# Kernel tuning notes

Hardware: AMD Instinct MI355X
Metric: run time of the kernel (lower is better)

The kernel has to match this reference:

```python
import jax, jax.numpy as jnp
import numpy as np

EXTENTS = (1, 2, 2)   # local half-window per (s, h, w) axis -> window 3x5x5 = 75
HEADS = 8
DIM_HEAD = 32
MASK_VALUE = -1e9


def unfold_axis(x, axis, size):
    # sliding windows of `size` along `axis` (stride 1), window dim appended last
    n = x.shape[axis] - size + 1
    idx = jnp.arange(n)[:, None] + jnp.arange(size)[None, :]
    out = jnp.take(x, idx, axis=axis)          # (..., n, size, ...)
    return jnp.moveaxis(out, axis + 1, -1)     # (..., n, ..., size)


def unfold3d(x, extents):
    # mimics torch x.unfold over dims 1,2,3; appends 3 window dims at the end
    for i in range(3):
        x = unfold_axis(x, i + 1, 2 * extents[i] + 1)
    return x


def local3d_attention(x, q, wq, wk, wv, wo, bo):
    b, s, h, w, dim = q.shape
    heads, dh = HEADS, DIM_HEAD
    inner = heads * dh
    scale = dh ** -0.5
    es, eh, ew = EXTENTS

    k = x @ wk.T                               # (b,s,h,w,inner)
    v = x @ wv.T
    qp = q @ wq.T

    pad_cfg = ((0, 0), (es, es), (eh, eh), (ew, ew), (0, 0))
    N = b * s * h * w
    # unfold -> (b,s,h,w,inner,ks,kh,kw); inner is head-major: (heads, dh)
    kwin = unfold3d(jnp.pad(k, pad_cfg), EXTENTS).reshape(N, heads, dh, -1)
    vwin = unfold3d(jnp.pad(v, pad_cfg), EXTENTS).reshape(N, heads, dh, -1)
    win = kwin.shape[-1]

    # mask: True where window position falls in the zero padding
    m = jnp.zeros((1, s, h, w), dtype=bool)
    m = jnp.pad(m, ((0, 0), (es, es), (eh, eh), (ew, ew)), constant_values=True)
    m = unfold3d(m, EXTENTS).reshape(s * h * w, win)
    m = jnp.tile(m, (b, 1))

    qn = qp.reshape(N, heads, dh)
    dots = jnp.einsum('nhd,nhdk->nhk', qn, kwin) * scale
    dots = jnp.where(m[:, None, :], MASK_VALUE, dots)
    attn = jax.nn.softmax(dots, axis=-1)
    out = jnp.einsum('nhk,nhdk->nhd', attn, vwin).reshape(b, s, h, w, inner)
    return out @ wo.T + bo                     # (b,s,h,w,dim)


def setup_inputs() -> dict:
    key = jax.random.key(0)
    ks = jax.random.split(key, 6)
    b, s, h, w, dim = 2, 8, 32, 16, 256
    inner = HEADS * DIM_HEAD
    sc_in = dim ** -0.5
    sc_out = inner ** -0.5
    return {
        'x': jax.random.normal(ks[0], (b, s, h, w, dim), jnp.float32),
        'q': jax.random.normal(ks[1], (b, s, h, w, dim), jnp.float32),
        'wq': jax.random.normal(ks[2], (inner, dim), jnp.float32) * sc_in,
        'wk': jax.random.normal(ks[3], (inner, dim), jnp.float32) * sc_in,
        'wv': jax.random.normal(ks[4], (inner, dim), jnp.float32) * sc_in,
        'wo': jax.random.normal(ks[5], (dim, inner), jnp.float32) * sc_out,
        'bo': jnp.zeros((dim,), jnp.float32),
    }


def reference(x, q, wq, wk, wv, wo, bo):
    return local3d_attention(x, q, wq, wk, wv, wo, bo)
```

## Files before the change

kernel.cpp:

```cpp
#include <hip/hip_runtime.h>
#include <hip/hip_bf16.h>
#include <math.h>

#define HEADS 8
#define DH 32
#define DIM 256
#define INNER 256
#define B_ 2
#define S_ 8
#define H_ 32
#define W_ 16
#define NTOK (B_*S_*H_*W_)

#define VHSTRIDE (512*32*16)
#define AOP 264

typedef _Float16 h16;
typedef h16 half8 __attribute__((ext_vector_type(8)));
typedef h16 half4 __attribute__((ext_vector_type(4)));
typedef float f32x4 __attribute__((ext_vector_type(4)));

#define QSCALE 0.17677669529663687f

#define GBM 128
#define GBN 64
#define GBK 32
#define GPITCH 40

__device__ __forceinline__ uint4 cvt8(const float4 a, const float4 b) {
    union { h16 h[8]; uint4 u; } p;
    p.h[0] = (h16)a.x; p.h[1] = (h16)a.y; p.h[2] = (h16)a.z; p.h[3] = (h16)a.w;
    p.h[4] = (h16)b.x; p.h[5] = (h16)b.y; p.h[6] = (h16)b.z; p.h[7] = (h16)b.w;
    return p.u;
}

template <int OUT_MODE>
__device__ __forceinline__ void mfma_gemm_tile_t(
    const float* __restrict__ A, const float* __restrict__ W,
    void* __restrict__ outv, int m0, int j0, float oscale,
    h16* aT, h16* bT)
{
    const int tid  = threadIdx.x;
    const int lane = tid & 63;
    const int wid  = tid >> 6;
    const int wr   = wid >> 1;
    const int wc   = wid & 1;
    const int r    = lane & 15;
    const int g    = lane >> 4;

    f32x4 acc[4][2];
    #pragma unroll
    for (int i = 0; i < 4; ++i)
        #pragma unroll
        for (int j = 0; j < 2; ++j)
            acc[i][j] = (f32x4){0.f, 0.f, 0.f, 0.f};

    const int arow  = tid >> 1;
    const int ahalf = (tid & 1) * 16;
    const int brow  = (tid & 127) >> 1;
    const bool doB  = tid < 128;

    for (int k0 = 0; k0 < DIM; k0 += GBK) {
        {
            const float* src = A + (size_t)(m0 + arow) * DIM + k0 + ahalf;
            const float4 u0 = *(const float4*)(src + 0);
            const float4 u1 = *(const float4*)(src + 4);
            const float4 u2 = *(const float4*)(src + 8);
            const float4 u3 = *(const float4*)(src + 12);
            *(uint4*)(aT + arow * GPITCH + ahalf + 0) = cvt8(u0, u1);
            *(uint4*)(aT + arow * GPITCH + ahalf + 8) = cvt8(u2, u3);
        }
        if (doB) {
            const float* src = W + (size_t)(j0 + brow) * DIM + k0 + ahalf;
            const float4 u0 = *(const float4*)(src + 0);
            const float4 u1 = *(const float4*)(src + 4);
            const float4 u2 = *(const float4*)(src + 8);
            const float4 u3 = *(const float4*)(src + 12);
            *(uint4*)(bT + brow * GPITCH + ahalf + 0) = cvt8(u0, u1);
            *(uint4*)(bT + brow * GPITCH + ahalf + 8) = cvt8(u2, u3);
        }
        __syncthreads();

        half8 af[4], bf[2];
        #pragma unroll
        for (int fr = 0; fr < 4; ++fr)
            af[fr] = *(const half8*)(aT + (wr * 64 + fr * 16 + r) * GPITCH + g * 8);
        #pragma unroll
        for (int fc = 0; fc < 2; ++fc)
            bf[fc] = *(const half8*)(bT + (wc * 32 + fc * 16 + r) * GPITCH + g * 8);

        #pragma unroll
        for (int fr = 0; fr < 4; ++fr)
            #pragma unroll
            for (int fc = 0; fc < 2; ++fc)
                acc[fr][fc] = __builtin_amdgcn_mfma_f32_16x16x32_f16(
                    af[fr], bf[fc], acc[fr][fc], 0, 0, 0);
        __syncthreads();
    }

    #pragma unroll
    for (int fr = 0; fr < 4; ++fr) {
        #pragma unroll
        for (int fc = 0; fc < 2; ++fc) {
            const int col = j0 + wc * 32 + fc * 16 + r;
            if constexpr (OUT_MODE == 4) {
                const int hd = col >> 5, d = col & 31;
                const int rowb = m0 + wr * 64 + fr * 16 + g * 4;
                union { h16 h[4]; uint2 u; } p;
                #pragma unroll
                for (int i = 0; i < 4; ++i) p.h[i] = (h16)(acc[fr][fc][i] * oscale);
                h16* dst = (h16*)outv + ((size_t)hd * 512 + (rowb >> 4)) * 512
                           + d * 16 + (rowb & 15);
                *(uint2*)dst = p.u;
            } else {
                const int hd = col >> 5, d = col & 31;
                #pragma unroll
                for (int i = 0; i < 4; ++i) {
                    const int row = m0 + wr * 64 + fr * 16 + g * 4 + i;
                    ((h16*)outv)[((size_t)hd * NTOK + row) * DH + d] =
                        (h16)(acc[fr][fc][i] * oscale);
                }
            }
        }
    }
}

__global__ __launch_bounds__(256) void proj_kernel(
    const float* __restrict__ x, const float* __restrict__ q,
    const float* __restrict__ wq, const float* __restrict__ wk,
    const float* __restrict__ wv, const float* __restrict__ wo,
    h16* __restrict__ qk, h16* __restrict__ vtb, h16* __restrict__ wof16)
{
    __shared__ h16 aT[GBM * GPITCH];
    __shared__ h16 bT[GBN * GPITCH];

    const int seg = blockIdx.y >> 2;
    const int jt  = blockIdx.y & 3;

    if (seg == 3) {
        const int idx = (blockIdx.x * 256 + threadIdx.x) * 4;
        const float4 v = *(const float4*)(wo + idx);
        union { h16 h[4]; uint2 u; } p;
        p.h[0] = (h16)v.x; p.h[1] = (h16)v.y;
        p.h[2] = (h16)v.z; p.h[3] = (h16)v.w;
        *(uint2*)(wof16 + idx) = p.u;
        return;
    }

    const float* A = (seg == 0) ? q : x;
    const float* W = (seg == 0) ? wq : ((seg == 1) ? wk : wv);

    if (seg == 2) {
        mfma_gemm_tile_t<4>(A, W, vtb, blockIdx.x * GBM, jt * GBN, 1.0f, aT, bT);
    } else {
        h16* outp = qk + (size_t)seg * HEADS * NTOK * DH;
        const float sc = (seg == 0) ? QSCALE : 1.0f;
        mfma_gemm_tile_t<3>(A, W, outp, blockIdx.x * GBM, jt * GBN, sc, aT, bT);
    }
}

__global__ __launch_bounds__(512, 4) void attn_kernel(
    const h16* __restrict__ qk, const h16* __restrict__ vtb,
    const h16* __restrict__ wof16, const float* __restrict__ bo,
    float* __restrict__ out)
{
    __shared__ h16 ao_lds[16][AOP];

    const int tid  = threadIdx.x;
    const int lane = tid & 63;
    const int wid  = __builtin_amdgcn_readfirstlane(tid >> 6);
    const int xr   = blockIdx.x;
    const int r    = ((xr & 7) << 6) | (xr >> 3);
    const int head = wid;
    const int h = r & 31, s = (r >> 5) & 7, b = r >> 8;
    const int n_base = r * 16;
    const int c = lane & 15, g = lane >> 4;

    const h16* qb = qk + (size_t)head * NTOK * DH;
    const h16* kb = qk + (size_t)(HEADS + head) * NTOK * DH;
    const h16* vb = vtb + (size_t)head * VHSTRIDE;

    int   tokb[16];
    float kill[16];
    #pragma unroll
    for (int t = 0; t < 16; ++t) {
        const int ds = t / 5, hh = t - 5 * ds;
        const int s2 = s + ds - 1;
        const int h2 = h + hh - 2;
        const bool inb = (t < 15) && ((unsigned)s2 < 8u) && ((unsigned)h2 < 32u);
        const int s2c = min(max(s2, 0), 7);
        const int h2c = min(max(h2, 0), 31);
        tokb[t] = ((b * 8 + s2c) * 32 + h2c) * 16;
        kill[t] = inb ? __builtin_inff() : -1e30f;
    }

    const half8 qf = *(const half8*)(qb + (size_t)(n_base + c) * DH + g * 8);

    f32x4 dots[16];
    #pragma unroll
    for (int t = 0; t < 16; ++t) {
        const half8 kf = *(const half8*)(kb + (size_t)(tokb[t] + c) * DH + g * 8);
        dots[t] = __builtin_amdgcn_mfma_f32_16x16x32_f16(
            kf, qf, (f32x4){0.f, 0.f, 0.f, 0.f}, 0, 0, 0);
    }

    union u2h4 { uint2 u2; half4 hv; } vpre[16];
    #pragma unroll
    for (int t = 0; t < 16; ++t) {
        const int bv = tokb[t] >> 4;
        vpre[t].u2 = *(const uint2*)(vb + (size_t)bv * 512 + c * 16 + 4 * g);
    }

    bool okw[4];
    #pragma unroll
    for (int i = 0; i < 4; ++i) {
        const int w2 = 4 * g + i;
        okw[i] = ((unsigned)(w2 - c + 2) <= 4u);
    }
    float mx = -1e30f;
    #pragma unroll
    for (int t = 0; t < 16; ++t) {
        const float kl = kill[t];
        #pragma unroll
        for (int i = 0; i < 4; ++i) {
            float dv = okw[i] ? dots[t][i] : -1e30f;
            dv = fminf(dv, kl);
            dots[t][i] = dv;
            mx = fmaxf(mx, dv);
        }
    }
    mx = fmaxf(mx, __shfl_xor(mx, 16));
    mx = fmaxf(mx, __shfl_xor(mx, 32));

    float sum = 0.f;
    int d0[16], d1[16];
    #pragma unroll
    for (int t = 0; t < 16; ++t) {
        const float e0v = __expf(dots[t][0] - mx);
        const float e1v = __expf(dots[t][1] - mx);
        const float e2v = __expf(dots[t][2] - mx);
        const float e3v = __expf(dots[t][3] - mx);
        sum += (e0v + e1v) + (e2v + e3v);
        union { h16 hh2[2]; int u; } p0, p1;
        p0.hh2[0] = (h16)e0v; p0.hh2[1] = (h16)e1v;
        p1.hh2[0] = (h16)e2v; p1.hh2[1] = (h16)e3v;
        d0[t] = p0.u; d1[t] = p1.u;
    }
    sum += __shfl_xor(sum, 16);
    sum += __shfl_xor(sum, 32);
    const float inv = 1.f / sum;
    float invq[4];
    #pragma unroll
    for (int i = 0; i < 4; ++i) invq[i] = __shfl(inv, 4 * g + i);

    f32x4 o0 = (f32x4){0.f,0.f,0.f,0.f};
    f32x4 o1 = (f32x4){0.f,0.f,0.f,0.f};
    #pragma unroll
    for (int t = 0; t < 16; ++t) {
        union { int u[2]; half4 hv; } pa;
        pa.u[0] = d0[t]; pa.u[1] = d1[t];

        const int bv = tokb[t] >> 4;
        union u2h4 v1;
        v1.u2 = *(const uint2*)(vb + (size_t)bv * 512 + (c + 16) * 16 + 4 * g);

        o0 = __builtin_amdgcn_mfma_f32_16x16x16f16(pa.hv, vpre[t].hv, o0, 0, 0, 0);
        o1 = __builtin_amdgcn_mfma_f32_16x16x16f16(pa.hv, v1.hv, o1, 0, 0, 0);
    }

    #pragma unroll
    for (int i = 0; i < 4; ++i) {
        ao_lds[4 * g + i][head * DH + c]      = (h16)(o0[i] * invq[i]);
        ao_lds[4 * g + i][head * DH + 16 + c] = (h16)(o1[i] * invq[i]);
    }
    __syncthreads();

    const int n0 = wid * 32;
    f32x4 oacc[2];
    oacc[0] = (f32x4){0.f,0.f,0.f,0.f};
    oacc[1] = (f32x4){0.f,0.f,0.f,0.f};
    #pragma unroll
    for (int kc = 0; kc < 8; ++kc) {
        const half8 af = *(const half8*)&ao_lds[c][kc * 32 + g * 8];
        #pragma unroll
        for (int nt = 0; nt < 2; ++nt) {
            const half8 bf = *(const half8*)(wof16
                + (size_t)(n0 + nt * 16 + c) * DIM + kc * 32 + g * 8);
            oacc[nt] = __builtin_amdgcn_mfma_f32_16x16x32_f16(af, bf, oacc[nt], 0, 0, 0);
        }
    }
    #pragma unroll
    for (int nt = 0; nt < 2; ++nt) {
        const int col = n0 + nt * 16 + c;
        const float badd = bo[col];
        #pragma unroll
        for (int i = 0; i < 4; ++i) {
            const int row = n_base + 4 * g + i;
            out[(size_t)row * INNER + col] = oacc[nt][i] + badd;
        }
    }
}

extern "C" void kernel_launch(void* const* d_in, const int* in_sizes, int n_in,
                              void* d_out, int out_size, void* d_ws, size_t ws_size,
                              hipStream_t stream) {
    const float* x  = (const float*)d_in[0];
    const float* q  = (const float*)d_in[1];
    const float* wq = (const float*)d_in[2];
    const float* wk = (const float*)d_in[3];
    const float* wv = (const float*)d_in[4];
    const float* wo = (const float*)d_in[5];
    const float* bo = (const float*)d_in[6];
    float* out = (float*)d_out;

    h16* qk    = (h16*)d_ws;
    h16* vtb   = qk + (size_t)2 * HEADS * NTOK * DH;
    h16* wof16 = vtb + (size_t)HEADS * VHSTRIDE;

    dim3 g1(NTOK / GBM, 13);
    proj_kernel<<<g1, 256, 0, stream>>>(x, q, wq, wk, wv, wo, qk, vtb, wof16);

    attn_kernel<<<512, 512, 0, stream>>>(qk, vtb, wof16, bo, out);
}
```

Baseline: 43.44 us.

## Retile projection GEMM to 64x256 blocks covering full output width

Each projection block now computes a 64-row by full 256-column output tile, so the A (activation) tile is read and converted only once per block instead of once per 64-column strip. The grid changes from 64x13 blocks to 128x4, and each wave now owns 64 columns with a 4x4 MFMA accumulator set. This cuts redundant global reads of x and q, but each block now loads the full 256-row weight slice every k-step, and the wo conversion segment uses narrower float2 loads. The added per-thread accumulator registers may also reduce occupancy.

```diff
diff --git a/kernel.cpp b/kernel.cpp
--- a/kernel.cpp
+++ b/kernel.cpp
@@ -22,10 +22,9 @@
 
 #define QSCALE 0.17677669529663687f
 
-#define GBM 128
-#define GBN 64
-#define GBK 32
 #define GPITCH 40
+#define PBM 64
+#define PBK 32
 
 __device__ __forceinline__ uint4 cvt8(const float4 a, const float4 b) {
     union { h16 h[8]; uint4 u; } p;
@@ -34,34 +33,49 @@
     return p.u;
 }
 
-template <int OUT_MODE>
-__device__ __forceinline__ void mfma_gemm_tile_t(
-    const float* __restrict__ A, const float* __restrict__ W,
-    void* __restrict__ outv, int m0, int j0, float oscale,
-    h16* aT, h16* bT)
+__global__ __launch_bounds__(256) void proj_kernel(
+    const float* __restrict__ x, const float* __restrict__ q,
+    const float* __restrict__ wq, const float* __restrict__ wk,
+    const float* __restrict__ wv, const float* __restrict__ wo,
+    h16* __restrict__ qk, h16* __restrict__ vtb, h16* __restrict__ wof16)
 {
-    const int tid  = threadIdx.x;
+    __shared__ h16 aT[PBM * GPITCH];
+    __shared__ h16 bT[256 * GPITCH];
+
+    const int seg = blockIdx.y;
+    const int tid = threadIdx.x;
+
+    if (seg == 3) {
+        const int idx = (blockIdx.x * 256 + tid) * 2;
+        const float2 v = *(const float2*)(wo + idx);
+        union { h16 h[2]; uint u; } p;
+        p.h[0] = (h16)v.x; p.h[1] = (h16)v.y;
+        *(uint*)(wof16 + idx) = p.u;
+        return;
+    }
+
+    const float* A = (seg == 0) ? q : x;
+    const float* W = (seg == 0) ? wq : ((seg == 1) ? wk : wv);
+    const float sc = (seg == 0) ? QSCALE : 1.0f;
+    const int m0 = blockIdx.x * PBM;
+
     const int lane = tid & 63;
     const int wid  = tid >> 6;
-    const int wr   = wid >> 1;
-    const int wc   = wid & 1;
     const int r    = lane & 15;
     const int g    = lane >> 4;
 
-    f32x4 acc[4][2];
+    f32x4 acc[4][4];
     #pragma unroll
     for (int i = 0; i < 4; ++i)
         #pragma unroll
-        for (int j = 0; j < 2; ++j)
+        for (int j = 0; j < 4; ++j)
             acc[i][j] = (f32x4){0.f, 0.f, 0.f, 0.f};
 
     const int arow  = tid >> 1;
     const int ahalf = (tid & 1) * 16;
-    const int brow  = (tid & 127) >> 1;
-    const bool doB  = tid < 128;
-
-    for (int k0 = 0; k0 < DIM; k0 += GBK) {
-        {
+
+    for (int k0 = 0; k0 < DIM; k0 += PBK) {
+        if (tid < 128) {
             const float* src = A + (size_t)(m0 + arow) * DIM + k0 + ahalf;
             const float4 u0 = *(const float4*)(src + 0);
             const float4 u1 = *(const float4*)(src + 4);
@@ -70,29 +84,35 @@
             *(uint4*)(aT + arow * GPITCH + ahalf + 0) = cvt8(u0, u1);
             *(uint4*)(aT + arow * GPITCH + ahalf + 8) = cvt8(u2, u3);
         }
-        if (doB) {
-            const float* src = W + (size_t)(j0 + brow) * DIM + k0 + ahalf;
+        {
+            const float* src = W + (size_t)tid * DIM + k0;
             const float4 u0 = *(const float4*)(src + 0);
             const float4 u1 = *(const float4*)(src + 4);
             const float4 u2 = *(const float4*)(src + 8);
             const float4 u3 = *(const float4*)(src + 12);
-            *(uint4*)(bT + brow * GPITCH + ahalf + 0) = cvt8(u0, u1);
-            *(uint4*)(bT + brow * GPITCH + ahalf + 8) = cvt8(u2, u3);
+            const float4 u4 = *(const float4*)(src + 16);
+            const float4 u5 = *(const float4*)(src + 20);
+            const float4 u6 = *(const float4*)(src + 24);
+            const float4 u7 = *(const float4*)(src + 28);
+            *(uint4*)(bT + tid * GPITCH + 0)  = cvt8(u0, u1);
+            *(uint4*)(bT + tid * GPITCH + 8)  = cvt8(u2, u3);
+            *(uint4*)(bT + tid * GPITCH + 16) = cvt8(u4, u5);
+            *(uint4*)(bT + tid * GPITCH + 24) = cvt8(u6, u7);
         }
         __syncthreads();
 
-        half8 af[4], bf[2];
+        half8 af[4], bf[4];
         #pragma unroll
         for (int fr = 0; fr < 4; ++fr)
-            af[fr] = *(const half8*)(aT + (wr * 64 + fr * 16 + r) * GPITCH + g * 8);
-        #pragma unroll
-        for (int fc = 0; fc < 2; ++fc)
-            bf[fc] = *(const half8*)(bT + (wc * 32 + fc * 16 + r) * GPITCH + g * 8);
+            af[fr] = *(const half8*)(aT + (fr * 16 + r) * GPITCH + g * 8);
+        #pragma unroll
+        for (int fc = 0; fc < 4; ++fc)
+            bf[fc] = *(const half8*)(bT + (wid * 64 + fc * 16 + r) * GPITCH + g * 8);
 
         #pragma unroll
         for (int fr = 0; fr < 4; ++fr)
             #pragma unroll
-            for (int fc = 0; fc < 2; ++fc)
+            for (int fc = 0; fc < 4; ++fc)
                 acc[fr][fc] = __builtin_amdgcn_mfma_f32_16x16x32_f16(
                     af[fr], bf[fc], acc[fr][fc], 0, 0, 0);
         __syncthreads();
@@ -101,61 +121,27 @@
     #pragma unroll
     for (int fr = 0; fr < 4; ++fr) {
         #pragma unroll
-        for (int fc = 0; fc < 2; ++fc) {
-            const int col = j0 + wc * 32 + fc * 16 + r;
-            if constexpr (OUT_MODE == 4) {
-                const int hd = col >> 5, d = col & 31;
-                const int rowb = m0 + wr * 64 + fr * 16 + g * 4;
+        for (int fc = 0; fc < 4; ++fc) {
+            const int col = wid * 64 + fc * 16 + r;
+            const int hd = col >> 5, d = col & 31;
+            if (seg == 2) {
+                const int rowb = m0 + fr * 16 + g * 4;
                 union { h16 h[4]; uint2 u; } p;
                 #pragma unroll
-                for (int i = 0; i < 4; ++i) p.h[i] = (h16)(acc[fr][fc][i] * oscale);
-                h16* dst = (h16*)outv + ((size_t)hd * 512 + (rowb >> 4)) * 512
+                for (int i = 0; i < 4; ++i) p.h[i] = (h16)acc[fr][fc][i];
+                h16* dst = vtb + ((size_t)hd * 512 + (rowb >> 4)) * 512
                            + d * 16 + (rowb & 15);
                 *(uint2*)dst = p.u;
             } else {
-                const int hd = col >> 5, d = col & 31;
+                h16* outp = qk + (size_t)seg * HEADS * NTOK * DH;
                 #pragma unroll
                 for (int i = 0; i < 4; ++i) {
-                    const int row = m0 + wr * 64 + fr * 16 + g * 4 + i;
-                    ((h16*)outv)[((size_t)hd * NTOK + row) * DH + d] =
-                        (h16)(acc[fr][fc][i] * oscale);
+                    const int row = m0 + fr * 16 + g * 4 + i;
+                    outp[((size_t)hd * NTOK + row) * DH + d] =
+                        (h16)(acc[fr][fc][i] * sc);
                 }
             }
         }
-    }
-}
-
-__global__ __launch_bounds__(256) void proj_kernel(
-    const float* __restrict__ x, const float* __restrict__ q,
-    const float* __restrict__ wq, const float* __restrict__ wk,
-    const float* __restrict__ wv, const float* __restrict__ wo,
-    h16* __restrict__ qk, h16* __restrict__ vtb, h16* __restrict__ wof16)
-{
-    __shared__ h16 aT[GBM * GPITCH];
-    __shared__ h16 bT[GBN * GPITCH];
-
-    const int seg = blockIdx.y >> 2;
-    const int jt  = blockIdx.y & 3;
-
-    if (seg == 3) {
-        const int idx = (blockIdx.x * 256 + threadIdx.x) * 4;
-        const float4 v = *(const float4*)(wo + idx);
-        union { h16 h[4]; uint2 u; } p;
-        p.h[0] = (h16)v.x; p.h[1] = (h16)v.y;
-        p.h[2] = (h16)v.z; p.h[3] = (h16)v.w;
-        *(uint2*)(wof16 + idx) = p.u;
-        return;
-    }
-
-    const float* A = (seg == 0) ? q : x;
-    const float* W = (seg == 0) ? wq : ((seg == 1) ? wk : wv);
-
-    if (seg == 2) {
-        mfma_gemm_tile_t<4>(A, W, vtb, blockIdx.x * GBM, jt * GBN, 1.0f, aT, bT);
-    } else {
-        h16* outp = qk + (size_t)seg * HEADS * NTOK * DH;
-        const float sc = (seg == 0) ? QSCALE : 1.0f;
-        mfma_gemm_tile_t<3>(A, W, outp, blockIdx.x * GBM, jt * GBN, sc, aT, bT);
     }
 }
 
@@ -317,7 +303,7 @@
     h16* vtb   = qk + (size_t)2 * HEADS * NTOK * DH;
     h16* wof16 = vtb + (size_t)HEADS * VHSTRIDE;
 
-    dim3 g1(NTOK / GBM, 13);
+    dim3 g1(NTOK / PBM, 4);
     proj_kernel<<<g1, 256, 0, stream>>>(x, q, wq, wk, wv, wo, qk, vtb, wof16);
 
     attn_kernel<<<512, 512, 0, stream>>>(qk, vtb, wof16, bo, out);
```

Measured after the change: 49.31 us. 13.5% more time.

## Double-buffer LDS and register-prefetch next K tile in projection GEMM

Applied to the files above, without the earlier changes.

The projection GEMM now uses two LDS buffers and loads the next K-slice from global memory into registers while MFMAs run on the current buffer, with the K loop fully unrolled. This hides global-load latency and drops one barrier per iteration. In exchange it doubles shared memory for the projection kernel and uses more registers, which can reduce occupancy.

```diff
diff --git a/kernel.cpp b/kernel.cpp
--- a/kernel.cpp
+++ b/kernel.cpp
@@ -35,10 +35,10 @@
 }
 
 template <int OUT_MODE>
-__device__ __forceinline__ void mfma_gemm_tile_t(
+__device__ __forceinline__ void mfma_gemm_dbuf(
     const float* __restrict__ A, const float* __restrict__ W,
     void* __restrict__ outv, int m0, int j0, float oscale,
-    h16* aT, h16* bT)
+    h16 (*aT)[GBM * GPITCH], h16 (*bT)[GBN * GPITCH])
 {
     const int tid  = threadIdx.x;
     const int lane = tid & 63;
@@ -60,34 +60,50 @@
     const int brow  = (tid & 127) >> 1;
     const bool doB  = tid < 128;
 
-    for (int k0 = 0; k0 < DIM; k0 += GBK) {
-        {
-            const float* src = A + (size_t)(m0 + arow) * DIM + k0 + ahalf;
-            const float4 u0 = *(const float4*)(src + 0);
-            const float4 u1 = *(const float4*)(src + 4);
-            const float4 u2 = *(const float4*)(src + 8);
-            const float4 u3 = *(const float4*)(src + 12);
-            *(uint4*)(aT + arow * GPITCH + ahalf + 0) = cvt8(u0, u1);
-            *(uint4*)(aT + arow * GPITCH + ahalf + 8) = cvt8(u2, u3);
-        }
+    const float* srcA = A + (size_t)(m0 + arow) * DIM + ahalf;
+    const float* srcB = W + (size_t)(j0 + brow) * DIM + ahalf;
+
+    float4 ra0, ra1, ra2, ra3, rb0, rb1, rb2, rb3;
+    ra0 = *(const float4*)(srcA + 0);  ra1 = *(const float4*)(srcA + 4);
+    ra2 = *(const float4*)(srcA + 8);  ra3 = *(const float4*)(srcA + 12);
+    if (doB) {
+        rb0 = *(const float4*)(srcB + 0);  rb1 = *(const float4*)(srcB + 4);
+        rb2 = *(const float4*)(srcB + 8);  rb3 = *(const float4*)(srcB + 12);
+    }
+
+    #pragma unroll
+    for (int p = 0; p < 8; ++p) {
+        h16* a = aT[p & 1];
+        h16* b = bT[p & 1];
+        *(uint4*)(a + arow * GPITCH + ahalf + 0) = cvt8(ra0, ra1);
+        *(uint4*)(a + arow * GPITCH + ahalf + 8) = cvt8(ra2, ra3);
         if (doB) {
-            const float* src = W + (size_t)(j0 + brow) * DIM + k0 + ahalf;
-            const float4 u0 = *(const float4*)(src + 0);
-            const float4 u1 = *(const float4*)(src + 4);
-            const float4 u2 = *(const float4*)(src + 8);
-            const float4 u3 = *(const float4*)(src + 12);
-            *(uint4*)(bT + brow * GPITCH + ahalf + 0) = cvt8(u0, u1);
-            *(uint4*)(bT + brow * GPITCH + ahalf + 8) = cvt8(u2, u3);
+            *(uint4*)(b + brow * GPITCH + ahalf + 0) = cvt8(rb0, rb1);
+            *(uint4*)(b + brow * GPITCH + ahalf + 8) = cvt8(rb2, rb3);
         }
         __syncthreads();
 
+        if (p < 7) {
+            const int k1 = (p + 1) * GBK;
+            ra0 = *(const float4*)(srcA + k1 + 0);
+            ra1 = *(const float4*)(srcA + k1 + 4);
+            ra2 = *(const float4*)(srcA + k1 + 8);
+            ra3 = *(const float4*)(srcA + k1 + 12);
+            if (doB) {
+                rb0 = *(const float4*)(srcB + k1 + 0);
+                rb1 = *(const float4*)(srcB + k1 + 4);
+                rb2 = *(const float4*)(srcB + k1 + 8);
+                rb3 = *(const float4*)(srcB + k1 + 12);
+            }
+        }
+
         half8 af[4], bf[2];
         #pragma unroll
         for (int fr = 0; fr < 4; ++fr)
-            af[fr] = *(const half8*)(aT + (wr * 64 + fr * 16 + r) * GPITCH + g * 8);
+            af[fr] = *(const half8*)(a + (wr * 64 + fr * 16 + r) * GPITCH + g * 8);
         #pragma unroll
         for (int fc = 0; fc < 2; ++fc)
-            bf[fc] = *(const half8*)(bT + (wc * 32 + fc * 16 + r) * GPITCH + g * 8);
+            bf[fc] = *(const half8*)(b + (wc * 32 + fc * 16 + r) * GPITCH + g * 8);
 
         #pragma unroll
         for (int fr = 0; fr < 4; ++fr)
@@ -95,7 +111,6 @@
             for (int fc = 0; fc < 2; ++fc)
                 acc[fr][fc] = __builtin_amdgcn_mfma_f32_16x16x32_f16(
                     af[fr], bf[fc], acc[fr][fc], 0, 0, 0);
-        __syncthreads();
     }
 
     #pragma unroll
@@ -131,8 +146,8 @@
     const float* __restrict__ wv, const float* __restrict__ wo,
     h16* __restrict__ qk, h16* __restrict__ vtb, h16* __restrict__ wof16)
 {
-    __shared__ h16 aT[GBM * GPITCH];
-    __shared__ h16 bT[GBN * GPITCH];
+    __shared__ h16 aT[2][GBM * GPITCH];
+    __shared__ h16 bT[2][GBN * GPITCH];
 
     const int seg = blockIdx.y >> 2;
     const int jt  = blockIdx.y & 3;
@@ -151,11 +166,11 @@
     const float* W = (seg == 0) ? wq : ((seg == 1) ? wk : wv);
 
     if (seg == 2) {
-        mfma_gemm_tile_t<4>(A, W, vtb, blockIdx.x * GBM, jt * GBN, 1.0f, aT, bT);
+        mfma_gemm_dbuf<4>(A, W, vtb, blockIdx.x * GBM, jt * GBN, 1.0f, aT, bT);
     } else {
         h16* outp = qk + (size_t)seg * HEADS * NTOK * DH;
         const float sc = (seg == 0) ? QSCALE : 1.0f;
-        mfma_gemm_tile_t<3>(A, W, outp, blockIdx.x * GBM, jt * GBN, sc, aT, bT);
+        mfma_gemm_dbuf<3>(A, W, outp, blockIdx.x * GBM, jt * GBN, sc, aT, bT);
     }
 }
 
```

After: 40.87 us. -5.9%, faster.
